# Optimization experiments

Measured on AMD Instinct MI355X. Metric: run time of the kernel, lower is better.

## Reference

```python
import jax, jax.numpy as jnp
import numpy as np

B, S, E, H = 4, 2048, 1024, 16
D = E // H  # head_dim = 64


def setup_inputs() -> dict:
    key = jax.random.key(0)
    ks = jax.random.split(key, 5)
    return {
        "x": jax.random.normal(ks[0], (B, S, E), dtype=jnp.float32),
        "w_qkv": jax.random.normal(ks[1], (3 * E, E), dtype=jnp.float32) * (E ** -0.5),
        "b_qkv": jax.random.normal(ks[2], (3 * E,), dtype=jnp.float32) * 0.02,
        "w_proj": jax.random.normal(ks[3], (E, E), dtype=jnp.float32) * (E ** -0.5),
        "b_proj": jax.random.normal(ks[4], (E,), dtype=jnp.float32) * 0.02,
    }


def reference(x, w_qkv, b_qkv, w_proj, b_proj):
    # fused QKV projection: [B,S,E] -> [B,S,3E] -> [B,S,3,H,D]
    qkv = (jnp.einsum("bse,fe->bsf", x, w_qkv) + b_qkv).reshape(B, S, 3, H, D)
    q, k, v = qkv[:, :, 0], qkv[:, :, 1], qkv[:, :, 2]  # each [B,S,H,D]
    scale = 1.0 / jnp.sqrt(jnp.asarray(D, dtype=q.dtype))
    scores = jnp.einsum("bqhd,bkhd->bhqk", q, k) * scale  # [B,H,S,S]
    attn = jax.nn.softmax(scores, axis=-1)
    out = jnp.einsum("bhqk,bkhd->bqhd", attn, v).reshape(B, S, E)
    return jnp.einsum("bse,fe->bsf", out, w_proj) + b_proj
```

## Files before the change

### kernel.cpp

```cpp
#include <hip/hip_runtime.h>
#include <cstdint>
#include <cstddef>

#define B_ 4
#define S_ 2048
#define E_ 1024
#define H_ 16
#define D_ 64
#define M_ (B_*S_)
#define NE_ ((size_t)B_*H_*S_*D_)

typedef unsigned int  u32;
typedef unsigned short u16;
typedef __attribute__((ext_vector_type(8))) short bf16x8;
typedef __attribute__((ext_vector_type(4))) float f32x4;

__device__ __forceinline__ u16 f2bf(float x) {
    u32 u = __float_as_uint(x);
    u32 r = (u + 0x7FFFu + ((u >> 16) & 1u)) >> 16;
    return (u16)r;
}
__device__ __forceinline__ float bf2f(u16 h) { return __uint_as_float((u32)h << 16); }

__device__ __forceinline__ u32 cvtpk_bf16(float lo, float hi) {
    u32 r;
    asm("v_cvt_pk_bf16_f32 %0, %1, %2" : "=v"(r) : "v"(lo), "v"(hi));
    return r;
}

__device__ __forceinline__ void gload_lds16(const void* gsrc, void* lds) {
    __builtin_amdgcn_global_load_lds(
        (const __attribute__((address_space(1))) u32*)gsrc,
        (__attribute__((address_space(3))) u32*)lds, 16, 0, 0);
}


__global__ __launch_bounds__(256)
void convert_img(const float* __restrict__ src, u16* __restrict__ dh, u16* __restrict__ dl)
{
    const int tile = blockIdx.x;
    const int nt = tile >> 4, kt = tile & 15;
    const size_t tb = (size_t)tile << 12;
    #pragma unroll
    for (int u = 0; u < 2; ++u) {
        const int ci = threadIdx.x + u * 256;
        const int r  = ci >> 3;
        const int c  = ci & 7;
        const float* s = src + ((size_t)(nt * 64 + r)) * 1024 + kt * 64 + c * 8;
        const float4 f0 = *(const float4*)s;
        const float4 f1 = *(const float4*)(s + 4);
        const float vals[8] = {f0.x, f0.y, f0.z, f0.w, f1.x, f1.y, f1.z, f1.w};
        __align__(16) short hs[8];
        __align__(16) short ls[8];
        #pragma unroll
        for (int j = 0; j < 8; ++j) {
            const u16 h = f2bf(vals[j]);
            hs[j] = (short)h;
            ls[j] = (short)f2bf(vals[j] - bf2f(h));
        }
        const size_t eoff = tb + r * 64 + ((size_t)(c ^ (r & 7)) << 3);
        *(bf16x8*)(dh + eoff) = *(const bf16x8*)hs;
        *(bf16x8*)(dl + eoff) = *(const bf16x8*)ls;
    }
}

template<int MODE>
__global__ __launch_bounds__(256)
void gemm_mfma(const u16* __restrict__ AIh, const u16* __restrict__ AIl,
               const u16* __restrict__ BIh, const u16* __restrict__ BIl,
               const float* __restrict__ bias, float* __restrict__ Cout,
               u16* __restrict__ qh, u16* __restrict__ ql,
               u16* __restrict__ kh,
               u16* __restrict__ vh, u16* __restrict__ vl)
{
    __shared__ __align__(16) u16 sA[2][2][4096];
    __shared__ __align__(16) u16 sB[2][2][4096];

    const int tid = threadIdx.x, lane = tid & 63, w = tid >> 6;
    const int quad = lane >> 4, l15 = lane & 15;
    const int m0  = blockIdx.x * 128;
    const int n0  = blockIdx.y * 128;
    const int mt0 = blockIdx.x * 2;
    const int nt0 = blockIdx.y * 2;
    const int rw  = w >> 1;
    const int cw  = w & 1;

    const int isB = w >> 1;
    const int sbw = w & 1;

    f32x4 acc[4][4];
    #pragma unroll
    for (int i = 0; i < 4; ++i)
        #pragma unroll
        for (int j = 0; j < 4; ++j)
            acc[i][j] = (f32x4){0.f, 0.f, 0.f, 0.f};

    for (int kt = 0; kt < 16; ++kt) {
        __syncthreads();
        {
            const size_t atile = ((size_t)((mt0 + sbw) * 16 + kt)) << 12;
            const size_t btile = ((size_t)((nt0 + sbw) * 16 + kt)) << 12;
            const u16* srcH = isB ? (BIh + btile) : (AIh + atile);
            const u16* srcL = isB ? (BIl + btile) : (AIl + atile);
            u16* dstH = isB ? &sB[sbw][0][0] : &sA[sbw][0][0];
            u16* dstL = isB ? &sB[sbw][1][0] : &sA[sbw][1][0];
            #pragma unroll
            for (int it = 0; it < 8; ++it)
                gload_lds16(srcH + it * 512 + lane * 8, dstH + it * 512);
            #pragma unroll
            for (int it = 0; it < 8; ++it)
                gload_lds16(srcL + it * 512 + lane * 8, dstL + it * 512);
        }
        __syncthreads();

        #pragma unroll
        for (int kk = 0; kk < 2; ++kk) {
            bf16x8 aH[4], aL[4], bH[4], bL[4];
            #pragma unroll
            for (int i = 0; i < 4; ++i) {
                const int r = i * 16 + l15;
                const int off = r * 64 + (((kk * 4 + quad) ^ (r & 7)) << 3);
                aH[i] = *(const bf16x8*)&sA[rw][0][off];
                aL[i] = *(const bf16x8*)&sA[rw][1][off];
            }
            #pragma unroll
            for (int j = 0; j < 4; ++j) {
                const int r = j * 16 + l15;
                const int off = r * 64 + (((kk * 4 + quad) ^ (r & 7)) << 3);
                bH[j] = *(const bf16x8*)&sB[cw][0][off];
                bL[j] = *(const bf16x8*)&sB[cw][1][off];
            }
            #pragma unroll
            for (int i = 0; i < 4; ++i)
                #pragma unroll
                for (int j = 0; j < 4; ++j) {
                    acc[i][j] = __builtin_amdgcn_mfma_f32_16x16x32_bf16(aL[i], bH[j], acc[i][j], 0, 0, 0);
                    acc[i][j] = __builtin_amdgcn_mfma_f32_16x16x32_bf16(aH[i], bL[j], acc[i][j], 0, 0, 0);
                    acc[i][j] = __builtin_amdgcn_mfma_f32_16x16x32_bf16(aH[i], bH[j], acc[i][j], 0, 0, 0);
                }
        }
    }

    const int fbase = n0 + cw * 64;
    float bj[4];
    #pragma unroll
    for (int j = 0; j < 4; ++j) bj[j] = bias[fbase + j * 16 + l15];

    if (MODE == 0) {
        const int cR = fbase >> 10;
        const int hh = (fbase >> 6) & 15;
        #pragma unroll
        for (int i = 0; i < 4; ++i)
            #pragma unroll
            for (int j = 0; j < 4; ++j)
                #pragma unroll
                for (int reg = 0; reg < 4; ++reg) {
                    float val = acc[i][j][reg] + bj[j];
                    const int m = m0 + rw * 64 + i * 16 + quad * 4 + reg;
                    const int d = j * 16 + l15;
                    const int bb = m >> 11, s = m & 2047;
                    const int bh = bb * 16 + hh;
                    if (cR == 0) val *= 0.125f;
                    const u16 h = f2bf(val);
                    if (cR == 0) {
                        const u16 lo = f2bf(val - bf2f(h));
                        const size_t idx = ((size_t)bh * 2048 + s) * 64 + d;
                        qh[idx] = h; ql[idx] = lo;
                    } else if (cR == 1) {
                        const size_t tile = (size_t)bh * 32 + (s >> 6);
                        const int r = s & 63;
                        const size_t off = (tile << 12) + r * 64 + (((d >> 3) ^ (r & 7)) << 3) + (d & 7);
                        kh[off] = h;
                    } else {
                        const u16 lo = f2bf(val - bf2f(h));
                        const size_t tile = (size_t)bh * 32 + (s >> 6);
                        const size_t off = (tile << 12) + d * 64 + ((((s & 63) >> 3) ^ (d & 7)) << 3) + (s & 7);
                        vh[off] = h; vl[off] = lo;
                    }
                }
    } else {
        #pragma unroll
        for (int i = 0; i < 4; ++i)
            #pragma unroll
            for (int j = 0; j < 4; ++j)
                #pragma unroll
                for (int reg = 0; reg < 4; ++reg) {
                    const int m = m0 + rw * 64 + i * 16 + quad * 4 + reg;
                    const int f = fbase + j * 16 + l15;
                    Cout[(size_t)m * 1024 + f] = acc[i][j][reg] + bj[j];
                }
    }
}

__global__ __launch_bounds__(256, 3)
void attn_mfma(const u16* __restrict__ qh, const u16* __restrict__ ql,
               const u16* __restrict__ kh,
               const u16* __restrict__ vh, const u16* __restrict__ vl,
               u16* __restrict__ oh, u16* __restrict__ ol)
{
    __shared__ __align__(16) u16 KV[3][4096];
    __shared__ __align__(16) u16 Psh[8192];

    const int tid  = threadIdx.x;
    const int lane = tid & 63, w = tid >> 6;
    const int quad = lane >> 4, l15 = lane & 15;
    const int bh = blockIdx.y;
    const int q0 = blockIdx.x * 128 + w * 32;

    bf16x8 Qf[2][2][2];
    #pragma unroll
    for (int qs = 0; qs < 2; ++qs)
        #pragma unroll
        for (int kk = 0; kk < 2; ++kk) {
            const size_t idx = ((size_t)bh * S_ + q0 + qs * 16 + l15) * 64 + kk * 32 + quad * 8;
            Qf[qs][kk][0] = *(const bf16x8*)(qh + idx);
            Qf[qs][kk][1] = *(const bf16x8*)(ql + idx);
        }

    f32x4 O[2][4];
    float l_part[2][4];
    #pragma unroll
    for (int qs = 0; qs < 2; ++qs)
        #pragma unroll
        for (int r = 0; r < 4; ++r) l_part[qs][r] = 0.f;
    #pragma unroll
    for (int qs = 0; qs < 2; ++qs)
        #pragma unroll
        for (int ds = 0; ds < 4; ++ds)
            O[qs][ds] = (f32x4){0.f, 0.f, 0.f, 0.f};

    const char* gk[3] = {(const char*)kh, (const char*)vh, (const char*)vl};

    for (int kt = 0; kt < S_ / 64; ++kt) {
        __syncthreads();
        const size_t tb = (((size_t)bh * 32 + kt) << 13);
        #pragma unroll
        for (int a = 0; a < 3; ++a)
            #pragma unroll
            for (int it = 0; it < 2; ++it) {
                const int off = w * 2048 + it * 1024;
                gload_lds16(gk[a] + tb + off + lane * 16, (char*)&KV[a][0] + off);
            }
        __syncthreads();

        f32x4 S[2][4];
        #pragma unroll
        for (int qs = 0; qs < 2; ++qs)
            #pragma unroll
            for (int ks = 0; ks < 4; ++ks)
                S[qs][ks] = (f32x4){-16.f, -16.f, -16.f, -16.f};

        __builtin_amdgcn_s_setprio(1);
        #pragma unroll
        for (int ks = 0; ks < 4; ++ks) {
            const int r = ks * 16 + l15;
            #pragma unroll
            for (int kk = 0; kk < 2; ++kk) {
                const int c = (kk * 4 + quad) ^ (r & 7);
                const bf16x8 Kh = *(const bf16x8*)&KV[0][r * 64 + c * 8];
                #pragma unroll
                for (int qs = 0; qs < 2; ++qs) {
                    S[qs][ks] = __builtin_amdgcn_mfma_f32_16x16x32_bf16(Qf[qs][kk][1], Kh, S[qs][ks], 0, 0, 0);
                    S[qs][ks] = __builtin_amdgcn_mfma_f32_16x16x32_bf16(Qf[qs][kk][0], Kh, S[qs][ks], 0, 0, 0);
                }
            }
        }
        __builtin_amdgcn_s_setprio(0);

        #pragma unroll
        for (int qs = 0; qs < 2; ++qs)
            #pragma unroll
            for (int reg = 0; reg < 4; ++reg) {
                float p[4];
                p[0] = __expf(S[qs][0][reg]);
                p[1] = __expf(S[qs][1][reg]);
                p[2] = __expf(S[qs][2][reg]);
                p[3] = __expf(S[qs][3][reg]);
                l_part[qs][reg] += (p[0] + p[1]) + (p[2] + p[3]);
                const int qloc = qs * 16 + quad * 4 + reg;
                const u32 r01 = cvtpk_bf16(p[0], p[1]);
                const u32 r23 = cvtpk_bf16(p[2], p[3]);
                u16* prow = &Psh[w * 2048 + qloc * 64 + (l15 & 7)];
                const int x  = l15 >> 3;
                const int s7 = qloc & 7;
                prow[((0 + x) ^ s7) * 8] = (u16)r01;
                prow[((2 + x) ^ s7) * 8] = (u16)(r01 >> 16);
                prow[((4 + x) ^ s7) * 8] = (u16)r23;
                prow[((6 + x) ^ s7) * 8] = (u16)(r23 >> 16);
            }

        __builtin_amdgcn_s_setprio(1);
        #pragma unroll
        for (int kk = 0; kk < 2; ++kk) {
            bf16x8 PhF[2];
            #pragma unroll
            for (int qs = 0; qs < 2; ++qs) {
                const int qrow = qs * 16 + l15;
                const int cph  = (kk * 4 + quad) ^ (qrow & 7);
                PhF[qs] = *(const bf16x8*)&Psh[w * 2048 + qrow * 64 + cph * 8];
            }
            #pragma unroll
            for (int ds = 0; ds < 4; ++ds) {
                const int r = ds * 16 + l15;
                const int c = (kk * 4 + quad) ^ (r & 7);
                const bf16x8 Vh = *(const bf16x8*)&KV[1][r * 64 + c * 8];
                const bf16x8 Vl = *(const bf16x8*)&KV[2][r * 64 + c * 8];
                #pragma unroll
                for (int qs = 0; qs < 2; ++qs) {
                    O[qs][ds] = __builtin_amdgcn_mfma_f32_16x16x32_bf16(PhF[qs], Vl, O[qs][ds], 0, 0, 0);
                    O[qs][ds] = __builtin_amdgcn_mfma_f32_16x16x32_bf16(PhF[qs], Vh, O[qs][ds], 0, 0, 0);
                }
            }
        }
        __builtin_amdgcn_s_setprio(0);
    }

    #pragma unroll
    for (int qs = 0; qs < 2; ++qs)
        #pragma unroll
        for (int reg = 0; reg < 4; ++reg) {
            float rs = l_part[qs][reg];
            rs += __shfl_xor(rs, 1, 16);
            rs += __shfl_xor(rs, 2, 16);
            rs += __shfl_xor(rs, 4, 16);
            rs += __shfl_xor(rs, 8, 16);
            l_part[qs][reg] = 1.f / rs;
        }

    const int bb = bh >> 4, hh = bh & 15;
    #pragma unroll
    for (int qs = 0; qs < 2; ++qs)
        #pragma unroll
        for (int reg = 0; reg < 4; ++reg) {
            const float inv = l_part[qs][reg];
            const int s = q0 + qs * 16 + quad * 4 + reg;
            const int m = bb * 2048 + s;
            const int mt = m >> 6, r = m & 63;
            const size_t tbase = ((size_t)(mt * 16 + hh)) << 12;
            #pragma unroll
            for (int ds = 0; ds < 4; ++ds) {
                const int d = ds * 16 + l15;
                const float val = O[qs][ds][reg] * inv;
                const u16 h  = f2bf(val);
                const u16 lo = f2bf(val - bf2f(h));
                const size_t off = tbase + r * 64 + (((d >> 3) ^ (r & 7)) << 3) + (d & 7);
                oh[off] = h; ol[off] = lo;
            }
        }
}

extern "C" void kernel_launch(void* const* d_in, const int* in_sizes, int n_in,
                              void* d_out, int out_size, void* d_ws, size_t ws_size,
                              hipStream_t stream) {
    const float* x      = (const float*)d_in[0];
    const float* w_qkv  = (const float*)d_in[1];
    const float* b_qkv  = (const float*)d_in[2];
    const float* w_proj = (const float*)d_in[3];
    const float* b_proj = (const float*)d_in[4];
    float* out = (float*)d_out;

    u16* qh  = (u16*)d_ws;
    u16* ql  = qh + NE_;
    u16* kh  = ql + NE_;
    u16* vh  = kh + NE_;
    u16* vl  = vh + NE_;
    u16* xh  = vl + NE_;
    u16* xl  = xh + NE_;
    u16* wqh = xl + NE_;
    u16* wql = wqh + (size_t)3 * 1024 * 1024;
    u16* oh  = xh;
    u16* ol  = xl;
    u16* wph = wqh;
    u16* wpl = wph + (size_t)1024 * 1024;

    convert_img<<<(M_ / 64) * 16, 256, 0, stream>>>(x, xh, xl);
    convert_img<<<48 * 16, 256, 0, stream>>>(w_qkv, wqh, wql);

    {
        dim3 grid(M_ / 128, (3 * E_) / 128);
        gemm_mfma<0><<<grid, 256, 0, stream>>>(xh, xl, wqh, wql,
                                               b_qkv, nullptr, qh, ql, kh, vh, vl);
    }
    {
        dim3 grid(S_ / 128, B_ * H_);
        attn_mfma<<<grid, 256, 0, stream>>>(qh, ql, kh, vh, vl, oh, ol);
    }
    convert_img<<<16 * 16, 256, 0, stream>>>(w_proj, wph, wpl);
    {
        dim3 grid(M_ / 128, E_ / 128);
        gemm_mfma<1><<<grid, 256, 0, stream>>>(oh, ol, wph, wpl,
                                               b_proj, out, nullptr, nullptr, nullptr,
                                               nullptr, nullptr);
    }
}
```

Before: 438.6 us.

## Keep softmax P in registers via transposed MFMA and permlane swaps

Swaps the MFMA operand order so S and O come out transposed, with each lane holding key/dim values for a single query. The probabilities can then be repacked into the PV operand layout with permlane32/16 swaps, which removes the LDS round-trip for P and its shared buffer. The Q scale is folded with log2(e) so exp2 is used, the row-sum reduction becomes two cross-lane shuffles, and the output is written as packed 8-byte stores. The risks are correctness of the permlane layout mapping and higher register pressure.

```diff
diff --git a/kernel.cpp b/kernel.cpp
--- a/kernel.cpp
+++ b/kernel.cpp
@@ -14,6 +14,7 @@
 typedef unsigned short u16;
 typedef __attribute__((ext_vector_type(8))) short bf16x8;
 typedef __attribute__((ext_vector_type(4))) float f32x4;
+typedef __attribute__((ext_vector_type(2))) unsigned int u32x2;
 
 __device__ __forceinline__ u16 f2bf(float x) {
     u32 u = __float_as_uint(x);
@@ -160,7 +161,7 @@
                     const int d = j * 16 + l15;
                     const int bb = m >> 11, s = m & 2047;
                     const int bh = bb * 16 + hh;
-                    if (cR == 0) val *= 0.125f;
+                    if (cR == 0) val *= 0.18033688011112042f;
                     const u16 h = f2bf(val);
                     if (cR == 0) {
                         const u16 lo = f2bf(val - bf2f(h));
@@ -199,7 +200,6 @@
                u16* __restrict__ oh, u16* __restrict__ ol)
 {
     __shared__ __align__(16) u16 KV[3][4096];
-    __shared__ __align__(16) u16 Psh[8192];
 
     const int tid  = threadIdx.x;
     const int lane = tid & 63, w = tid >> 6;
@@ -218,11 +218,7 @@
         }
 
     f32x4 O[2][4];
-    float l_part[2][4];
-    #pragma unroll
-    for (int qs = 0; qs < 2; ++qs)
-        #pragma unroll
-        for (int r = 0; r < 4; ++r) l_part[qs][r] = 0.f;
+    float l_part[2] = {0.f, 0.f};
     #pragma unroll
     for (int qs = 0; qs < 2; ++qs)
         #pragma unroll
@@ -248,7 +244,8 @@
         for (int qs = 0; qs < 2; ++qs)
             #pragma unroll
             for (int ks = 0; ks < 4; ++ks)
-                S[qs][ks] = (f32x4){-16.f, -16.f, -16.f, -16.f};
+                S[qs][ks] = (f32x4){-23.083120654223414f, -23.083120654223414f,
+                                    -23.083120654223414f, -23.083120654223414f};
 
         __builtin_amdgcn_s_setprio(1);
         #pragma unroll
@@ -260,45 +257,49 @@
                 const bf16x8 Kh = *(const bf16x8*)&KV[0][r * 64 + c * 8];
                 #pragma unroll
                 for (int qs = 0; qs < 2; ++qs) {
-                    S[qs][ks] = __builtin_amdgcn_mfma_f32_16x16x32_bf16(Qf[qs][kk][1], Kh, S[qs][ks], 0, 0, 0);
-                    S[qs][ks] = __builtin_amdgcn_mfma_f32_16x16x32_bf16(Qf[qs][kk][0], Kh, S[qs][ks], 0, 0, 0);
+                    S[qs][ks] = __builtin_amdgcn_mfma_f32_16x16x32_bf16(Kh, Qf[qs][kk][1], S[qs][ks], 0, 0, 0);
+                    S[qs][ks] = __builtin_amdgcn_mfma_f32_16x16x32_bf16(Kh, Qf[qs][kk][0], S[qs][ks], 0, 0, 0);
                 }
             }
         }
         __builtin_amdgcn_s_setprio(0);
 
-        #pragma unroll
-        for (int qs = 0; qs < 2; ++qs)
-            #pragma unroll
-            for (int reg = 0; reg < 4; ++reg) {
-                float p[4];
-                p[0] = __expf(S[qs][0][reg]);
-                p[1] = __expf(S[qs][1][reg]);
-                p[2] = __expf(S[qs][2][reg]);
-                p[3] = __expf(S[qs][3][reg]);
-                l_part[qs][reg] += (p[0] + p[1]) + (p[2] + p[3]);
-                const int qloc = qs * 16 + quad * 4 + reg;
-                const u32 r01 = cvtpk_bf16(p[0], p[1]);
-                const u32 r23 = cvtpk_bf16(p[2], p[3]);
-                u16* prow = &Psh[w * 2048 + qloc * 64 + (l15 & 7)];
-                const int x  = l15 >> 3;
-                const int s7 = qloc & 7;
-                prow[((0 + x) ^ s7) * 8] = (u16)r01;
-                prow[((2 + x) ^ s7) * 8] = (u16)(r01 >> 16);
-                prow[((4 + x) ^ s7) * 8] = (u16)r23;
-                prow[((6 + x) ^ s7) * 8] = (u16)(r23 >> 16);
-            }
+        u32 PA[2][2][4];
+        #pragma unroll
+        for (int qs = 0; qs < 2; ++qs) {
+            float lsum = 0.f;
+            u32 PK[4][2];
+            #pragma unroll
+            for (int ks = 0; ks < 4; ++ks) {
+                const float p0 = __builtin_exp2f(S[qs][ks][0]);
+                const float p1 = __builtin_exp2f(S[qs][ks][1]);
+                const float p2 = __builtin_exp2f(S[qs][ks][2]);
+                const float p3 = __builtin_exp2f(S[qs][ks][3]);
+                lsum += (p0 + p1) + (p2 + p3);
+                PK[ks][0] = cvtpk_bf16(p0, p1);
+                PK[ks][1] = cvtpk_bf16(p2, p3);
+            }
+            l_part[qs] += lsum;
+            #pragma unroll
+            for (int kk = 0; kk < 2; ++kk) {
+                const u32x2 t0 = __builtin_amdgcn_permlane32_swap(PK[2 * kk][0], PK[2 * kk + 1][0], false, false);
+                const u32x2 w02 = __builtin_amdgcn_permlane16_swap(t0.x, t0.y, false, false);
+                const u32x2 t1 = __builtin_amdgcn_permlane32_swap(PK[2 * kk][1], PK[2 * kk + 1][1], false, false);
+                const u32x2 w13 = __builtin_amdgcn_permlane16_swap(t1.x, t1.y, false, false);
+                PA[qs][kk][0] = w02.x;
+                PA[qs][kk][1] = w13.x;
+                PA[qs][kk][2] = w02.y;
+                PA[qs][kk][3] = w13.y;
+            }
+        }
 
         __builtin_amdgcn_s_setprio(1);
         #pragma unroll
         for (int kk = 0; kk < 2; ++kk) {
-            bf16x8 PhF[2];
-            #pragma unroll
-            for (int qs = 0; qs < 2; ++qs) {
-                const int qrow = qs * 16 + l15;
-                const int cph  = (kk * 4 + quad) ^ (qrow & 7);
-                PhF[qs] = *(const bf16x8*)&Psh[w * 2048 + qrow * 64 + cph * 8];
-            }
+            union { u32 w4[4]; bf16x8 v; } pu0, pu1;
+            #pragma unroll
+            for (int c = 0; c < 4; ++c) { pu0.w4[c] = PA[0][kk][c]; pu1.w4[c] = PA[1][kk][c]; }
+            const bf16x8 paf[2] = {pu0.v, pu1.v};
             #pragma unroll
             for (int ds = 0; ds < 4; ++ds) {
                 const int r = ds * 16 + l15;
@@ -307,46 +308,51 @@
                 const bf16x8 Vl = *(const bf16x8*)&KV[2][r * 64 + c * 8];
                 #pragma unroll
                 for (int qs = 0; qs < 2; ++qs) {
-                    O[qs][ds] = __builtin_amdgcn_mfma_f32_16x16x32_bf16(PhF[qs], Vl, O[qs][ds], 0, 0, 0);
-                    O[qs][ds] = __builtin_amdgcn_mfma_f32_16x16x32_bf16(PhF[qs], Vh, O[qs][ds], 0, 0, 0);
+                    O[qs][ds] = __builtin_amdgcn_mfma_f32_16x16x32_bf16(Vl, paf[qs], O[qs][ds], 0, 0, 0);
+                    O[qs][ds] = __builtin_amdgcn_mfma_f32_16x16x32_bf16(Vh, paf[qs], O[qs][ds], 0, 0, 0);
                 }
             }
         }
         __builtin_amdgcn_s_setprio(0);
     }
 
-    #pragma unroll
-    for (int qs = 0; qs < 2; ++qs)
-        #pragma unroll
-        for (int reg = 0; reg < 4; ++reg) {
-            float rs = l_part[qs][reg];
-            rs += __shfl_xor(rs, 1, 16);
-            rs += __shfl_xor(rs, 2, 16);
-            rs += __shfl_xor(rs, 4, 16);
-            rs += __shfl_xor(rs, 8, 16);
-            l_part[qs][reg] = 1.f / rs;
-        }
+    float linv[2];
+    #pragma unroll
+    for (int qs = 0; qs < 2; ++qs) {
+        float rs = l_part[qs];
+        rs += __shfl_xor(rs, 16);
+        rs += __shfl_xor(rs, 32);
+        linv[qs] = 1.f / rs;
+    }
 
     const int bb = bh >> 4, hh = bh & 15;
     #pragma unroll
-    for (int qs = 0; qs < 2; ++qs)
-        #pragma unroll
-        for (int reg = 0; reg < 4; ++reg) {
-            const float inv = l_part[qs][reg];
-            const int s = q0 + qs * 16 + quad * 4 + reg;
-            const int m = bb * 2048 + s;
-            const int mt = m >> 6, r = m & 63;
-            const size_t tbase = ((size_t)(mt * 16 + hh)) << 12;
-            #pragma unroll
-            for (int ds = 0; ds < 4; ++ds) {
-                const int d = ds * 16 + l15;
-                const float val = O[qs][ds][reg] * inv;
-                const u16 h  = f2bf(val);
-                const u16 lo = f2bf(val - bf2f(h));
-                const size_t off = tbase + r * 64 + (((d >> 3) ^ (r & 7)) << 3) + (d & 7);
-                oh[off] = h; ol[off] = lo;
-            }
-        }
+    for (int qs = 0; qs < 2; ++qs) {
+        const float inv = linv[qs];
+        const int s = q0 + qs * 16 + l15;
+        const int m = bb * 2048 + s;
+        const int mt = m >> 6, r = m & 63;
+        const size_t tbase = ((size_t)(mt * 16 + hh)) << 12;
+        #pragma unroll
+        for (int ds = 0; ds < 4; ++ds) {
+            const int d0 = ds * 16 + quad * 4;
+            const float v0 = O[qs][ds][0] * inv;
+            const float v1 = O[qs][ds][1] * inv;
+            const float v2 = O[qs][ds][2] * inv;
+            const float v3 = O[qs][ds][3] * inv;
+            const u32 h01 = cvtpk_bf16(v0, v1);
+            const u32 h23 = cvtpk_bf16(v2, v3);
+            const float r0 = v0 - bf2f((u16)h01);
+            const float r1 = v1 - bf2f((u16)(h01 >> 16));
+            const float r2 = v2 - bf2f((u16)h23);
+            const float r3 = v3 - bf2f((u16)(h23 >> 16));
+            const u32 l01 = cvtpk_bf16(r0, r1);
+            const u32 l23 = cvtpk_bf16(r2, r3);
+            const size_t off = tbase + r * 64 + (size_t)((((d0 >> 3) ^ (r & 7)) << 3) + (d0 & 7));
+            *(u32x2*)(oh + off) = (u32x2){h01, h23};
+            *(u32x2*)(ol + off) = (u32x2){l01, l23};
+        }
+    }
 }
 
 extern "C" void kernel_launch(void* const* d_in, const int* in_sizes, int n_in,
```

After: 438.9 us. No clear change (+0.1%).
